# Performance work log

Measured on AMD Instinct MI355X. Metric: run time of the kernel, lower is better.

Reference implementation:

```python
import jax, jax.numpy as jnp
import numpy as np
import math

B = 1; SEQ = 2048; CHUNK = 16; K = SEQ // CHUNK
DIM = 1024; NH = 16; HD = DIM // NH
NL = 2; NLF = 2; HID = 4096; VOCAB = 32000; CSP_MAX = 4
EPS = 1e-5
BS = CHUNK + 2                 # per-chunk decoder block: [fx, sep, tokens]
L = K * BS + 2                 # + trailing [fx_last, sep]


def rope_cache(n_pos, n_elem, base=10000.0):
    theta = 1.0 / (base ** (jnp.arange(0, n_elem, 2, dtype=jnp.float32) / n_elem))
    idx = jnp.outer(jnp.arange(n_pos, dtype=jnp.float32), theta)  # [n_pos, n_elem/2]
    cos = jnp.concatenate([jnp.cos(idx), jnp.cos(idx)], -1)
    sin = jnp.concatenate([jnp.sin(idx), jnp.sin(idx)], -1)
    return cos, sin  # [n_pos, n_elem]


def apply_rope(x, cos, sin):
    # x: [b, h, l, d]; cos/sin: [l, d] (rope_n_elem == head_dim)
    h = x.shape[-1] // 2
    rot = jnp.concatenate([-x[..., h:], x[..., :h]], -1)
    return x * cos + rot * sin


def rmsnorm(x, w):
    return x * jax.lax.rsqrt(jnp.mean(x * x, -1, keepdims=True) + EPS) * w


def attention(x, wqkv, wo, cos, sin, mask):
    b, l, d = x.shape
    qkv = (x @ wqkv).reshape(b, l, 3, NH, HD).transpose(2, 0, 3, 1, 4)
    q, k, v = qkv[0], qkv[1], qkv[2]            # [b, h, l, hd]
    q = apply_rope(q, cos, sin)
    k = apply_rope(k, cos, sin)
    s = jnp.einsum('bhqd,bhkd->bhqk', q, k) / math.sqrt(HD)
    if mask is not None:
        s = jnp.where(mask, s, jnp.float32(-1e30))
    o = jnp.einsum('bhqk,bhkd->bhqd', jax.nn.softmax(s, -1), v)
    return o.transpose(0, 2, 1, 3).reshape(b, l, d) @ wo


def block(x, ln1, wqkv, wo, ln2, wg, wu, wd, cos, sin, mask):
    x = x + attention(rmsnorm(x, ln1), wqkv, wo, cos, sin, mask)
    h = rmsnorm(x, ln2)
    return x + (jax.nn.silu(h @ wg) * (h @ wu)) @ wd


def cat_mask(n, bs):
    # CAT mask: (kv divides block-start | same block) & causal
    q = jnp.arange(n)[:, None]
    kv = jnp.arange(n)[None, :]
    return ((kv % bs == 0) | (q // bs == kv // bs)) & (q >= kv)


def setup_inputs() -> dict:
    key = jax.random.key(0)
    ks = jax.random.split(key, 24)
    w = lambda k, s: jax.random.normal(k, s, jnp.float32) * 0.02
    return {
        'input_ids': jax.random.randint(ks[0], (B, SEQ), 0, VOCAB, dtype=jnp.int32),
        'chunk_size_power': 4,
        'f_wte': w(ks[1], (VOCAB, DIM)), 'f_pos': w(ks[2], (SEQ, DIM)),
        'f_adapt': w(ks[3], (CSP_MAX + 1, DIM)),
        'f_ln1': jnp.ones((NLF, DIM)), 'f_ln2': jnp.ones((NLF, DIM)),
        'f_wqkv': w(ks[4], (NLF, DIM, 3 * DIM)), 'f_wo': w(ks[5], (NLF, DIM, DIM)),
        'f_wg': w(ks[6], (NLF, DIM, HID)), 'f_wu': w(ks[7], (NLF, DIM, HID)),
        'f_wd': w(ks[8], (NLF, HID, DIM)),
        'f_norm': jnp.ones((DIM,)), 'f_proj': w(ks[9], (DIM, CHUNK * DIM)),
        'dummy_fx': w(ks[10], (CSP_MAX + 1, DIM)), 'wte': w(ks[11], (VOCAB, DIM)),
        'sep': w(ks[12], (1, DIM)),
        'd_ln1': jnp.ones((NL, DIM)), 'd_ln2': jnp.ones((NL, DIM)),
        'd_wqkv': w(ks[13], (NL, DIM, 3 * DIM)), 'd_wo': w(ks[14], (NL, DIM, DIM)),
        'd_wg': w(ks[15], (NL, DIM, HID)), 'd_wu': w(ks[16], (NL, DIM, HID)),
        'd_wd': w(ks[17], (NL, HID, DIM)),
        'd_norm': jnp.ones((DIM,)), 'w_out': w(ks[18], (VOCAB, DIM)),
    }


def reference(input_ids, chunk_size_power, f_wte, f_pos, f_adapt, f_ln1, f_ln2,
              f_wqkv, f_wo, f_wg, f_wu, f_wd, f_norm, f_proj, dummy_fx, wte, sep,
              d_ln1, d_ln2, d_wqkv, d_wo, d_wg, d_wu, d_wd, d_norm, w_out):
    csp = int(chunk_size_power)
    ids = input_ids.reshape(B, K, CHUNK)
    cosf, sinf = rope_cache(2 + CHUNK, HD)

    def compress(ids_c, chunk_idx):
        # ids_c: [B, CHUNK] (one chunk, vmapped over K)
        x = f_wte[ids_c]
        adaptive = jnp.broadcast_to(f_adapt[csp], (B, 1, DIM))
        pos_tok = jnp.broadcast_to(f_pos[chunk_idx], (B, 1, DIM))
        x = jnp.concatenate([adaptive, pos_tok, x], 1)  # [B, CHUNK+2, DIM]
        for i in range(NLF):
            x = block(x, f_ln1[i], f_wqkv[i], f_wo[i], f_ln2[i],
                      f_wg[i], f_wu[i], f_wd[i], cosf, sinf, None)
        x = rmsnorm(x, f_norm)[:, 2:, :].reshape(B, CHUNK * DIM)
        # chunk_size_power == log2(CHUNK): bilinear interpolate to same size == identity
        return x @ f_proj.T  # [B, DIM]

    fx = jax.vmap(compress, in_axes=(1, 0), out_axes=1)(ids, jnp.arange(K))  # [B, K, DIM]

    fx_last = fx[:, -1:, :]
    dummy = jnp.broadcast_to(dummy_fx[csp], (B, 1, DIM))
    fx_sh = jnp.concatenate([dummy, fx[:, :-1, :]], 1)[:, :, None, :]  # [B, K, 1, DIM]
    sep_t = jnp.broadcast_to(sep[0], (B, K, 1, DIM))
    emb = wte[ids]  # [B, K, CHUNK, DIM]
    x = jnp.concatenate([fx_sh, sep_t, emb], 2).reshape(B, K * BS, DIM)
    x = jnp.concatenate([x, fx_last, jnp.broadcast_to(sep[0], (B, 1, DIM))], 1)  # [B, L, DIM]

    # per-block repeating RoPE positions (cache built for len BS, tiled)
    pos = jnp.tile(jnp.arange(BS), K + 1)[:L]
    cosb, sinb = rope_cache(BS, HD)
    cosd, sind = cosb[pos], sinb[pos]
    mask = cat_mask(L, BS)

    for i in range(NL):
        x = block(x, d_ln1[i], d_wqkv[i], d_wo[i], d_ln2[i],
                  d_wg[i], d_wu[i], d_wd[i], cosd, sind, mask)
    x = rmsnorm(x, d_norm)
    return x @ w_out.T  # [B, L, VOCAB]
```

## Files before the change

kernel.cpp:

```cpp
#include <hip/hip_runtime.h>
#include <math.h>

#define L_DEC 2306
#define MPAD 2560
#define T_FINE 2304

typedef float f32x4 __attribute__((ext_vector_type(4)));
typedef __bf16 bf16x8 __attribute__((ext_vector_type(8)));
typedef unsigned short u16;
typedef unsigned short us4 __attribute__((ext_vector_type(4)));
typedef unsigned short us8 __attribute__((ext_vector_type(8)));

#define GLOAD16(g, l) __builtin_amdgcn_global_load_lds( \
    (const __attribute__((address_space(1))) unsigned int*)(g), \
    (__attribute__((address_space(3))) unsigned int*)(l), 16, 0, 0)

__device__ __forceinline__ u16 f2bf(float f) {
  unsigned u = __float_as_uint(f);
  u += 0x7fffu + ((u >> 16) & 1u);
  return (u16)(u >> 16);
}

__device__ __forceinline__ int fix_csp(const int* p) {
  int c = p[0];
  if ((unsigned)c <= 4u) return c;
  float f = __uint_as_float((unsigned)c);
  int c2 = (int)f;
  return ((unsigned)c2 <= 4u) ? c2 : 4;
}

__device__ __forceinline__ void xcd_map(int gx, int gy, int& bm, int& bn, int TS) {
  const int nwg = gx * gy;
  const int orig = blockIdx.y * gx + blockIdx.x;
  const int q8 = nwg >> 3, r8 = nwg & 7;
  const int xcd = orig & 7, idx8 = orig >> 3;
  const int wg = (xcd < r8 ? xcd * (q8 + 1) : r8 * (q8 + 1) + (xcd - r8) * q8) + idx8;
  bm = (wg / gx) * TS;
  bn = (wg % gx) * TS;
}

template<int EPI>
__global__ __launch_bounds__(512, 1) void k_gemm3(const u16* __restrict__ A,
                                                  const u16* __restrict__ B,
                                                  float* __restrict__ C,
                                                  int N, int K, int Mstore)
{
  extern __shared__ u16 lds[];
  const int tid = threadIdx.x;
  int bm, bn; xcd_map(gridDim.x, gridDim.y, bm, bn, 256);
  const int w = tid >> 6, lane = tid & 63;
  const int wm = (w >> 2) * 128, wn = (w & 3) * 64;
  const int lr = lane & 15, kh = lane >> 4;

#define STAGE3(buf, kt) do {                                                   \
    u16* lA = lds + (buf) * 32768;                                             \
    u16* lB = lA + 16384;                                                      \
    _Pragma("unroll")                                                          \
    for (int p = 0; p < 4; ++p) {                                              \
      int e = p * 512 + tid;                                                   \
      int row = e >> 3;                                                        \
      int kc = ((e & 7) ^ (row & 7)) * 8;    \
      GLOAD16(A + (size_t)(bm + row) * K + (size_t)(kt) * 64 + kc, lA + e * 8);\
      GLOAD16(B + (size_t)(bn + row) * K + (size_t)(kt) * 64 + kc, lB + e * 8);\
    }                                                                          \
  } while (0)

  f32x4 acc[8][4] = {};
  const int nt = K >> 6;
  STAGE3(0, 0);
  __syncthreads();
  int cur = 0;
  for (int t = 0; t < nt; ++t) {
    if (t + 1 < nt) STAGE3(cur ^ 1, t + 1);
    const u16* pA = lds + cur * 32768;
    const u16* pB = pA + 16384;
    const int xr = (lr & 7) << 3;
#pragma unroll
    for (int kt2 = 0; kt2 < 2; ++kt2) {
      bf16x8 af[8], bf[4];
#pragma unroll
      for (int m = 0; m < 8; ++m)
        af[m] = *(const bf16x8*)&pA[(wm + m * 16 + lr) * 64 + ((kt2 * 32 + kh * 8) ^ xr)];
#pragma unroll
      for (int n = 0; n < 4; ++n)
        bf[n] = *(const bf16x8*)&pB[(wn + n * 16 + lr) * 64 + ((kt2 * 32 + kh * 8) ^ xr)];
#pragma unroll
      for (int m = 0; m < 8; ++m)
#pragma unroll
        for (int n = 0; n < 4; ++n)
          acc[m][n] = __builtin_amdgcn_mfma_f32_16x16x32_bf16(af[m], bf[n], acc[m][n], 0, 0, 0);
    }
    __syncthreads();
    cur ^= 1;
  }
#undef STAGE3

#pragma unroll
  for (int m = 0; m < 8; ++m) {
    int gr0 = bm + wm + m * 16 + kh * 4;
#pragma unroll
    for (int n = 0; n < 4; ++n) {
      int gc = bn + wn + n * 16 + lr;
#pragma unroll
      for (int r = 0; r < 4; ++r) {
        int gr = gr0 + r;
        if (gr < Mstore) C[(size_t)gr * N + gc] = acc[m][n][r];
      }
    }
  }
}

template<int EPI>
__global__ __launch_bounds__(512, 1) void k_gemm2(const u16* __restrict__ A,
                                                  const u16* __restrict__ B,
                                                  float* __restrict__ C,
                                                  u16* __restrict__ Cb,
                                                  int N, int K, int Mstore)
{
  __shared__ u16 As[2][8192];
  __shared__ u16 Bs[2][8192];
  const int tid = threadIdx.x;
  int bm, bn; xcd_map(gridDim.x, gridDim.y, bm, bn, 256);
  const int w = tid >> 6, lane = tid & 63;
  const int wm = (w >> 2) * 128, wn = (w & 3) * 64;
  const int lr = lane & 15, kh = lane >> 4;
  const int r0 = tid >> 2;
  const int ksrc = 8 * ((tid & 3) ^ ((tid >> 3) & 3));
  const u16* ga = A + (size_t)(bm + r0) * K + ksrc;
  const u16* gb = B + (size_t)(bn + r0) * K + ksrc;
  const size_t rstep = (size_t)128 * K;
  const int cola = (kh * 8) ^ (((lr >> 1) & 3) << 3);

#define STAGE2(buf, kt) do {                                   \
    const u16* gA = ga + (size_t)(kt) * 32;                    \
    const u16* gB = gb + (size_t)(kt) * 32;                    \
    GLOAD16(gA,         &As[buf][tid * 8]);                    \
    GLOAD16(gA + rstep, &As[buf][tid * 8 + 4096]);             \
    GLOAD16(gB,         &Bs[buf][tid * 8]);                    \
    GLOAD16(gB + rstep, &Bs[buf][tid * 8 + 4096]);             \
  } while (0)

  f32x4 acc[8][4] = {};
  const int nt = K >> 5;
  STAGE2(0, 0);
  __syncthreads();
  int cur = 0;
  for (int t = 0; t < nt; ++t) {
    if (t + 1 < nt) STAGE2(cur ^ 1, t + 1);
    bf16x8 af[8], bf[4];
#pragma unroll
    for (int m = 0; m < 8; ++m)
      af[m] = *(const bf16x8*)&As[cur][(wm + m * 16 + lr) * 32 + cola];
#pragma unroll
    for (int n = 0; n < 4; ++n)
      bf[n] = *(const bf16x8*)&Bs[cur][(wn + n * 16 + lr) * 32 + cola];
#pragma unroll
    for (int m = 0; m < 8; ++m)
#pragma unroll
      for (int n = 0; n < 4; ++n)
        acc[m][n] = __builtin_amdgcn_mfma_f32_16x16x32_bf16(af[m], bf[n], acc[m][n], 0, 0, 0);
    __syncthreads();
    cur ^= 1;
  }
#undef STAGE2

#pragma unroll
  for (int m = 0; m < 8; ++m) {
    int gr0 = bm + wm + m * 16 + kh * 4;
#pragma unroll
    for (int n = 0; n < 4; ++n) {
      int gc = bn + wn + n * 16 + lr;
#pragma unroll
      for (int r = 0; r < 4; ++r) {
        int gr = gr0 + r;
        if (gr < Mstore) C[(size_t)gr * N + gc] = acc[m][n][r];
      }
    }
  }
}

template<int EPI>
__global__ __launch_bounds__(256) void k_gemm_bt(const u16* __restrict__ A,
                                                 const u16* __restrict__ B,
                                                 float* __restrict__ C,
                                                 u16* __restrict__ Cb,
                                                 int N, int K, int Mstore, int kchunk)
{
  __shared__ u16 As[4096];
  __shared__ u16 Bs[4096];
  const int tid = threadIdx.x;
  int bm, bn; xcd_map(gridDim.x, gridDim.y, bm, bn, 128);
  const int k0 = blockIdx.z * kchunk;
  const int w = tid >> 6, lane = tid & 63;
  const int wm = (w >> 1) * 64, wn = (w & 1) * 64;
  const int lr = lane & 15, kh = lane >> 4;
  const int r0 = tid >> 2;
  const int ksrc = 8 * ((tid & 3) ^ ((tid >> 3) & 3));
  const int cola = (kh * 8) ^ (((lr >> 1) & 3) << 3);

  const u16* ga = A + (size_t)(bm + r0) * K + k0 + ksrc;
  const u16* gb = B + (size_t)(bn + r0) * K + k0 + ksrc;
  u16* la = &As[tid * 8];
  u16* lb = &Bs[tid * 8];
  const size_t rstep = (size_t)64 * K;

  f32x4 acc[4][4] = {};
  for (int kk = 0; kk < kchunk; kk += 32) {
    GLOAD16(ga, la); GLOAD16(ga + rstep, la + 2048);
    GLOAD16(gb, lb); GLOAD16(gb + rstep, lb + 2048);
    ga += 32; gb += 32;
    __syncthreads();
    bf16x8 af[4], bfr[4];
#pragma unroll
    for (int m = 0; m < 4; ++m)
      af[m] = *(const bf16x8*)&As[(wm + m * 16 + lr) * 32 + cola];
#pragma unroll
    for (int n = 0; n < 4; ++n)
      bfr[n] = *(const bf16x8*)&Bs[(wn + n * 16 + lr) * 32 + cola];
#pragma unroll
    for (int m = 0; m < 4; ++m)
#pragma unroll
      for (int n = 0; n < 4; ++n)
        acc[m][n] = __builtin_amdgcn_mfma_f32_16x16x32_bf16(af[m], bfr[n], acc[m][n], 0, 0, 0);
    __syncthreads();
  }

  float* Cz = (EPI == 0) ? C + (size_t)blockIdx.z * Mstore * N : C;
  const int N2 = N >> 1;
#pragma unroll
  for (int m = 0; m < 4; ++m) {
    int gr0 = bm + wm + m * 16 + kh * 4;
#pragma unroll
    for (int n = 0; n < 4; ++n) {
      int gc = bn + wn + n * 16 + lr;
#pragma unroll
      for (int r = 0; r < 4; ++r) {
        int gr = gr0 + r;
        if (EPI == 2) {
          float x = acc[m][n][r];
          float px = __shfl_xor(x, 1);
          if (!(lr & 1) && gr < Mstore) {
            float s = x / (1.f + expf(-x)) * px;
            Cb[(size_t)gr * N2 + (gc >> 1)] = f2bf(s);
          }
        } else if (gr < Mstore) {
          size_t off = (size_t)gr * N + gc;
          if (EPI == 0) Cz[off] = acc[m][n][r];
          else          C[off] += acc[m][n][r];
        }
      }
    }
  }
}

__global__ __launch_bounds__(256) void k_gemm_hf(const u16* __restrict__ A,
                                                 const float* __restrict__ B,
                                                 float* __restrict__ C,
                                                 int N, int K, int Mstore)
{
  __shared__ u16 As[4096];
  __shared__ u16 Bs[4096];
  const int tid = threadIdx.x;
  const int bm = blockIdx.y * 128, bn = blockIdx.x * 128;
  const int w = tid >> 6, lane = tid & 63;
  const int wm = (w >> 1) * 64, wn = (w & 1) * 64;
  const int lr = lane & 15, kh = lane >> 4;
  const int r0 = tid >> 2;
  const int ksrc = 8 * ((tid & 3) ^ ((tid >> 3) & 3));
  const int cola = (kh * 8) ^ (((lr >> 1) & 3) << 3);
  const u16* ga = A + (size_t)(bm + r0) * K + ksrc;
  u16* la = &As[tid * 8];
  const size_t rstep = (size_t)64 * K;

  f32x4 acc[4][4] = {};
  for (int kk = 0; kk < K; kk += 32) {
    GLOAD16(ga, la); GLOAD16(ga + rstep, la + 2048);
    ga += 32;
#pragma unroll
    for (int p = 0; p < 4; ++p) {
      int e = tid + p * 256;
      int row = e >> 3, kc = (e & 7) * 4;
      int kcs = kc ^ (((row >> 1) & 3) << 3);
      float4 v = *(const float4*)(B + (size_t)(bn + row) * K + kk + kc);
      us4 pk; pk[0] = f2bf(v.x); pk[1] = f2bf(v.y); pk[2] = f2bf(v.z); pk[3] = f2bf(v.w);
      *(us4*)&Bs[row * 32 + kcs] = pk;
    }
    __syncthreads();
    bf16x8 af[4], bfr[4];
#pragma unroll
    for (int m = 0; m < 4; ++m)
      af[m] = *(const bf16x8*)&As[(wm + m * 16 + lr) * 32 + cola];
#pragma unroll
    for (int n = 0; n < 4; ++n)
      bfr[n] = *(const bf16x8*)&Bs[(wn + n * 16 + lr) * 32 + cola];
#pragma unroll
    for (int m = 0; m < 4; ++m)
#pragma unroll
      for (int n = 0; n < 4; ++n)
        acc[m][n] = __builtin_amdgcn_mfma_f32_16x16x32_bf16(af[m], bfr[n], acc[m][n], 0, 0, 0);
    __syncthreads();
  }
#pragma unroll
  for (int m = 0; m < 4; ++m) {
    int gr0 = bm + wm + m * 16 + kh * 4;
#pragma unroll
    for (int n = 0; n < 4; ++n) {
      int gc = bn + wn + n * 16 + lr;
#pragma unroll
      for (int r = 0; r < 4; ++r) {
        int gr = gr0 + r;
        if (gr < Mstore) C[(size_t)gr * N + gc] = acc[m][n][r];
      }
    }
  }
}

__global__ __launch_bounds__(256) void k_wt2(const float* __restrict__ W, u16* __restrict__ Wt,
                                             int K, int N, int rs, int ro) {
  __shared__ u16 t[64][80];
  int n0 = blockIdx.x * 64, k0 = blockIdx.y * 64;
#pragma unroll
  for (int p = 0; p < 4; ++p) {
    int id = threadIdx.x + p * 256;
    int row = id >> 4, c4 = (id & 15) * 4;
    float4 v = *(const float4*)(W + (size_t)(k0 + row) * N + n0 + c4);
    t[c4 + 0][row] = f2bf(v.x);
    t[c4 + 1][row] = f2bf(v.y);
    t[c4 + 2][row] = f2bf(v.z);
    t[c4 + 3][row] = f2bf(v.w);
  }
  __syncthreads();
#pragma unroll
  for (int p = 0; p < 2; ++p) {
    int id = threadIdx.x + p * 256;
    int row = id >> 3, c8 = (id & 7) * 8;
    *(us8*)(Wt + ((size_t)(n0 + row) * rs + ro) * K + k0 + c8) = *(const us8*)&t[row][c8];
  }
}

__global__ void k_cvt(const float* __restrict__ x, u16* __restrict__ y, int n4) {
  for (int i = blockIdx.x * 256 + threadIdx.x; i < n4; i += gridDim.x * 256) {
    float4 v = ((const float4*)x)[i];
    us4 p; p[0] = f2bf(v.x); p[1] = f2bf(v.y); p[2] = f2bf(v.z); p[3] = f2bf(v.w);
    ((us4*)y)[i] = p;
  }
}

__global__ void k_reduce_add(const float* __restrict__ p, float* __restrict__ dst,
                             int n, int planes, int addDst) {
  for (int i = blockIdx.x * 256 + threadIdx.x; i < n; i += gridDim.x * 256) {
    float s = addDst ? dst[i] : 0.f;
    for (int z = 0; z < planes; ++z) s += p[(size_t)z * n + i];
    dst[i] = s;
  }
}

__global__ void k_rope_table(float* __restrict__ cosT, float* __restrict__ sinT) {
  int i = blockIdx.x * blockDim.x + threadIdx.x;
  if (i >= 18 * 64) return;
  int p = i >> 6, d = i & 63;
  float theta = powf(10000.f, -(float)(d & 31) / 32.f);
  float ang = (float)p * theta;
  cosT[i] = cosf(ang);
  sinT[i] = sinf(ang);
}

__global__ void k_fine_embed(const int* __restrict__ ids, const int* __restrict__ cspp,
                             const float* __restrict__ f_wte, const float* __restrict__ f_pos,
                             const float* __restrict__ f_adapt, float* __restrict__ xF) {
  int csp = fix_csp(cspp);
  for (int idx = blockIdx.x * 256 + threadIdx.x; idx < T_FINE * 1024; idx += gridDim.x * 256) {
    int r = idx >> 10, d = idx & 1023;
    int c = r / 18, j = r - c * 18;
    float v;
    if (j == 0)      v = f_adapt[csp * 1024 + d];
    else if (j == 1) v = f_pos[c * 1024 + d];
    else             v = f_wte[(size_t)ids[c * 16 + j - 2] * 1024 + d];
    xF[idx] = v;
  }
}

__global__ __launch_bounds__(256) void k_rmsnorm_bf(const float* __restrict__ x,
                                                    const float* __restrict__ w,
                                                    u16* __restrict__ y) {
  int t = blockIdx.x;
  const float4 v = *(const float4*)(x + (size_t)t * 1024 + threadIdx.x * 4);
  float ss = v.x * v.x + v.y * v.y + v.z * v.z + v.w * v.w;
#pragma unroll
  for (int off = 32; off; off >>= 1) ss += __shfl_xor(ss, off);
  __shared__ float ps[4];
  if ((threadIdx.x & 63) == 0) ps[threadIdx.x >> 6] = ss;
  __syncthreads();
  float inv = rsqrtf((ps[0] + ps[1] + ps[2] + ps[3]) * (1.f / 1024.f) + 1e-5f);
  const float4 wv = *(const float4*)(w + threadIdx.x * 4);
  us4 o;
  o[0] = f2bf(v.x * inv * wv.x); o[1] = f2bf(v.y * inv * wv.y);
  o[2] = f2bf(v.z * inv * wv.z); o[3] = f2bf(v.w * inv * wv.w);
  *(us4*)(y + (size_t)t * 1024 + threadIdx.x * 4) = o;
}

__global__ __launch_bounds__(256) void k_rmsnorm_pack_bf(const float* __restrict__ x,
                                                         const float* __restrict__ w,
                                                         u16* __restrict__ y) {
  int b = blockIdx.x;
  int c = b >> 4, r = b & 15;
  const float* xr = x + (size_t)(c * 18 + 2 + r) * 1024;
  const float4 v = *(const float4*)(xr + threadIdx.x * 4);
  float ss = v.x * v.x + v.y * v.y + v.z * v.z + v.w * v.w;
#pragma unroll
  for (int off = 32; off; off >>= 1) ss += __shfl_xor(ss, off);
  __shared__ float ps[4];
  if ((threadIdx.x & 63) == 0) ps[threadIdx.x >> 6] = ss;
  __syncthreads();
  float inv = rsqrtf((ps[0] + ps[1] + ps[2] + ps[3]) * (1.f / 1024.f) + 1e-5f);
  const float4 wv = *(const float4*)(w + threadIdx.x * 4);
  us4 o;
  o[0] = f2bf(v.x * inv * wv.x); o[1] = f2bf(v.y * inv * wv.y);
  o[2] = f2bf(v.z * inv * wv.z); o[3] = f2bf(v.w * inv * wv.w);
  *(us4*)(y + (size_t)b * 1024 + threadIdx.x * 4) = o;
}

__global__ __launch_bounds__(256) void k_rope(float* __restrict__ qkv,
                                              const float* __restrict__ cosT,
                                              const float* __restrict__ sinT) {
  int t = blockIdx.x;
  int p = t % 18;
  float* row = qkv + (size_t)t * 3072;
#pragma unroll
  for (int i = 0; i < 4; ++i) {
    int it = threadIdx.x + i * 256;
    int s = it >> 9, rem = it & 511, h = rem >> 5, d = rem & 31;
    float* px = row + s * 1024 + h * 64 + d;
    float x1 = px[0], x2 = px[32];
    float cv = cosT[p * 64 + d], sv = sinT[p * 64 + d];
    px[0]  = x1 * cv - x2 * sv;
    px[32] = x2 * cv + x1 * sv;
  }
}

__global__ __launch_bounds__(256) void k_attn_fine2(const float* __restrict__ qkv,
                                                    u16* __restrict__ out) {
  __shared__ float q[4][18][68], k[4][18][68], v[4][18][68], s[4][18][20];
  int c = blockIdx.x;
  int w = threadIdx.x >> 6, lane = threadIdx.x & 63;
  int h = blockIdx.y * 4 + w;
  const float* base = qkv + (size_t)c * 18 * 3072 + h * 64;
#pragma unroll 3
  for (int r = 0; r < 18; ++r) {
    q[w][r][lane] = base[(size_t)r * 3072 + lane];
    k[w][r][lane] = base[(size_t)r * 3072 + 1024 + lane];
    v[w][r][lane] = base[(size_t)r * 3072 + 2048 + lane];
  }
  __syncthreads();
#pragma unroll
  for (int it = 0; it < 6; ++it) {
    int idx = lane + it * 64;
    if (idx < 324) {
      int qi = (idx * 3641) >> 16;
      int ki = idx - qi * 18;
      const float* qr = q[w][qi];
      const float* kr = k[w][ki];
      float a = 0.f;
#pragma unroll
      for (int d = 0; d < 64; d += 4) {
        float4 x = *(const float4*)&qr[d];
        float4 y = *(const float4*)&kr[d];
        a += x.x * y.x + x.y * y.y + x.z * y.z + x.w * y.w;
      }
      s[w][qi][ki] = a * 0.125f;
    }
  }
  __syncthreads();
  if (lane < 18) {
    float mx = -1e30f;
#pragma unroll
    for (int j = 0; j < 18; ++j) mx = fmaxf(mx, s[w][lane][j]);
    float sum = 0.f;
#pragma unroll
    for (int j = 0; j < 18; ++j) { float e = expf(s[w][lane][j] - mx); s[w][lane][j] = e; sum += e; }
    float inv = 1.f / sum;
#pragma unroll
    for (int j = 0; j < 18; ++j) s[w][lane][j] *= inv;
  }
  __syncthreads();
  float vcol[18];
#pragma unroll
  for (int ki = 0; ki < 18; ++ki) vcol[ki] = v[w][ki][lane];
#pragma unroll 2
  for (int qi = 0; qi < 18; ++qi) {
    float o = 0.f;
#pragma unroll
    for (int ki = 0; ki < 18; ++ki) o += s[w][qi][ki] * vcol[ki];
    out[(size_t)(c * 18 + qi) * 1024 + h * 64 + lane] = f2bf(o);
  }
}

__global__ __launch_bounds__(512) void k_attn_dec3(const float* __restrict__ qkv,
                                                   u16* __restrict__ out) {
  extern __shared__ float dyn[];
  float* Kl = dyn;
  float* Vl = Kl + 146 * 65;
  float* Ql = Vl + 146 * 65;
  float* Sw = Ql + 18 * 65;
  const int bq = blockIdx.x, h = blockIdx.y;
  const int w = threadIdx.x >> 6, lane = threadIdx.x & 63;
  const int t0 = 18 * bq;
  const int nq = (bq < 128) ? 18 : 2;
  const int nstage = (bq < 128) ? (bq + 18) : 130;

  {
    int rr = threadIdx.x >> 2, c = threadIdx.x & 3;
    for (int row = rr; row < nstage; row += 128) {
      int kv = (row <= bq) ? 18 * row : t0 + (row - bq);
      const float* kp = qkv + (size_t)kv * 3072 + 1024 + h * 64 + c * 16;
#pragma unroll
      for (int q4 = 0; q4 < 4; ++q4) {
        float4 a = *(const float4*)(kp + q4 * 4);
        float4 b = *(const float4*)(kp + 1024 + q4 * 4);
        int d = c * 16 + q4 * 4;
        float* kd = Kl + row * 65 + d;
        float* vd = Vl + row * 65 + d;
        kd[0] = a.x; kd[1] = a.y; kd[2] = a.z; kd[3] = a.w;
        vd[0] = b.x; vd[1] = b.y; vd[2] = b.z; vd[3] = b.w;
      }
    }
    if (rr < nq) {
      const float* qp = qkv + (size_t)(t0 + rr) * 3072 + h * 64 + c * 16;
#pragma unroll
      for (int q4 = 0; q4 < 4; ++q4) {
        float4 a = *(const float4*)(qp + q4 * 4);
        int d = c * 16 + q4 * 4;
        float* qd = Ql + rr * 65 + d;
        qd[0] = a.x; qd[1] = a.y; qd[2] = a.z; qd[3] = a.w;
      }
    }
  }
  __syncthreads();

  for (int r = w; r < nq; r += 8) {
    const int nk = bq + 1 + r;
    float* S = Sw + w * 148;
    const float* qr = Ql + r * 65;
    float mx = -1e30f;
    for (int i = lane; i < nk; i += 64) {
      const float* kr = Kl + i * 65;
      float a = 0.f;
#pragma unroll
      for (int d = 0; d < 64; ++d) a += qr[d] * kr[d];
      a *= 0.125f;
      S[i] = a;
      mx = fmaxf(mx, a);
    }
#pragma unroll
    for (int off = 32; off; off >>= 1) mx = fmaxf(mx, __shfl_xor(mx, off));
    float sum = 0.f;
    for (int i = lane; i < nk; i += 64) { float e = expf(S[i] - mx); S[i] = e; sum += e; }
#pragma unroll
    for (int off = 32; off; off >>= 1) sum += __shfl_xor(sum, off);
    float inv = 1.f / sum;
    __builtin_amdgcn_wave_barrier();
    float o = 0.f;
    for (int i = 0; i < nk; ++i) o += S[i] * Vl[i * 65 + lane];
    out[(size_t)(t0 + r) * 1024 + h * 64 + lane] = f2bf(o * inv);
  }
}

__global__ __launch_bounds__(256) void k_attn_dec2(const float* __restrict__ qkv,
                                                   u16* __restrict__ out) {
  __shared__ float sc_s[4][160];
  int t = blockIdx.x;
  int w = threadIdx.x >> 6, lane = threadIdx.x & 63;
  int h = blockIdx.y * 4 + w;
  float* sc = sc_s[w];
  int bq = t / 18;
  int nstart = bq + 1;
  int nown = t - 18 * bq;
  int nk = nstart + nown;
  int g = lane >> 2, j = lane & 3;
  const float* qb = qkv + (size_t)t * 3072 + h * 64 + j * 16;
  float4 q0 = *(const float4*)(qb);
  float4 q1 = *(const float4*)(qb + 4);
  float4 q2 = *(const float4*)(qb + 8);
  float4 q3 = *(const float4*)(qb + 12);
  for (int i0 = 0; i0 < nk; i0 += 16) {
    int i = i0 + g;
    float p = 0.f;
    if (i < nk) {
      int kv = (i < nstart) ? 18 * i : 18 * bq + (i - nstart) + 1;
      const float* kp = qkv + (size_t)kv * 3072 + 1024 + h * 64 + j * 16;
      float4 k0 = *(const float4*)(kp);
      float4 k1 = *(const float4*)(kp + 4);
      float4 k2 = *(const float4*)(kp + 8);
      float4 k3 = *(const float4*)(kp + 12);
      p = q0.x * k0.x + q0.y * k0.y + q0.z * k0.z + q0.w * k0.w
        + q1.x * k1.x + q1.y * k1.y + q1.z * k1.z + q1.w * k1.w
        + q2.x * k2.x + q2.y * k2.y + q2.z * k2.z + q2.w * k2.w
        + q3.x * k3.x + q3.y * k3.y + q3.z * k3.z + q3.w * k3.w;
    }
    p += __shfl_xor(p, 1);
    p += __shfl_xor(p, 2);
    if (i < nk && j == 0) sc[i] = p * 0.125f;
  }
  __syncthreads();
  float mx = -1e30f;
  for (int i = lane; i < nk; i += 64) mx = fmaxf(mx, sc[i]);
#pragma unroll
  for (int off = 32; off; off >>= 1) mx = fmaxf(mx, __shfl_xor(mx, off));
  float sum = 0.f;
  for (int i = lane; i < nk; i += 64) { float e = expf(sc[i] - mx); sc[i] = e; sum += e; }
#pragma unroll
  for (int off = 32; off; off >>= 1) sum += __shfl_xor(sum, off);
  float inv = 1.f / sum;
  __syncthreads();
  const float* vb = qkv + 2048 + h * 64 + lane;
  float o0 = 0.f, o1 = 0.f, o2 = 0.f, o3 = 0.f;
  int i = 0;
  for (; i + 4 <= nk; i += 4) {
    int ia = i, ib = i + 1, ic = i + 2, id = i + 3;
    int kva = (ia < nstart) ? 18 * ia : 18 * bq + (ia - nstart) + 1;
    int kvb = (ib < nstart) ? 18 * ib : 18 * bq + (ib - nstart) + 1;
    int kvc = (ic < nstart) ? 18 * ic : 18 * bq + (ic - nstart) + 1;
    int kvd = (id < nstart) ? 18 * id : 18 * bq + (id - nstart) + 1;
    o0 += sc[ia] * vb[(size_t)kva * 3072];
    o1 += sc[ib] * vb[(size_t)kvb * 3072];
    o2 += sc[ic] * vb[(size_t)kvc * 3072];
    o3 += sc[id] * vb[(size_t)kvd * 3072];
  }
  for (; i < nk; ++i) {
    int kv = (i < nstart) ? 18 * i : 18 * bq + (i - nstart) + 1;
    o0 += sc[i] * vb[(size_t)kv * 3072];
  }
  float o = (o0 + o1) + (o2 + o3);
  out[(size_t)t * 1024 + h * 64 + lane] = f2bf(o * inv);
}

__global__ void k_assemble(const int* __restrict__ ids, const int* __restrict__ cspp,
                           const float* __restrict__ fx, const float* __restrict__ dummy_fx,
                           const float* __restrict__ sep, const float* __restrict__ wte,
                           float* __restrict__ xD) {
  int csp = fix_csp(cspp);
  for (int idx = blockIdx.x * 256 + threadIdx.x; idx < MPAD * 1024; idx += gridDim.x * 256) {
    int t = idx >> 10, d = idx & 1023;
    float v;
    if (t >= L_DEC)     v = 0.f;
    else if (t == 2305) v = sep[d];
    else if (t == 2304) v = fx[127 * 1024 + d];
    else {
      int k = t / 18, r = t - k * 18;
      if (r == 0)      v = (k == 0) ? dummy_fx[csp * 1024 + d] : fx[(k - 1) * 1024 + d];
      else if (r == 1) v = sep[d];
      else             v = wte[(size_t)ids[k * 16 + r - 2] * 1024 + d];
    }
    xD[idx] = v;
  }
}

extern "C" void kernel_launch(void* const* d_in, const int* in_sizes, int n_in,
                              void* d_out, int out_size, void* d_ws, size_t ws_size,
                              hipStream_t stream) {
  const int*   input_ids = (const int*)d_in[0];
  const int*   cspp      = (const int*)d_in[1];
  const float* f_wte     = (const float*)d_in[2];
  const float* f_pos     = (const float*)d_in[3];
  const float* f_adapt   = (const float*)d_in[4];
  const float* f_ln1     = (const float*)d_in[5];
  const float* f_ln2     = (const float*)d_in[6];
  const float* f_wqkv    = (const float*)d_in[7];
  const float* f_wo      = (const float*)d_in[8];
  const float* f_wg      = (const float*)d_in[9];
  const float* f_wu      = (const float*)d_in[10];
  const float* f_wd      = (const float*)d_in[11];
  const float* f_norm    = (const float*)d_in[12];
  const float* f_proj    = (const float*)d_in[13];
  const float* dummy_fx  = (const float*)d_in[14];
  const float* wte       = (const float*)d_in[15];
  const float* sep       = (const float*)d_in[16];
  const float* d_ln1     = (const float*)d_in[17];
  const float* d_ln2     = (const float*)d_in[18];
  const float* d_wqkv    = (const float*)d_in[19];
  const float* d_wo      = (const float*)d_in[20];
  const float* d_wg      = (const float*)d_in[21];
  const float* d_wu      = (const float*)d_in[22];
  const float* d_wd      = (const float*)d_in[23];
  const float* d_norm    = (const float*)d_in[24];
  const float* w_out     = (const float*)d_in[25];

  float* cosT = (float*)d_ws;
  float* sinT = cosT + 1152;
  u16*   bufH = (u16*)(sinT + 1152);
  u16*   w_outb = bufH + (size_t)MPAD * 1024;
  const size_t WS_NEED = 2 * 1152 * 4 + (size_t)MPAD * 1024 * 2 + (size_t)32000 * 1024 * 2;
  const bool big_ws = ws_size >= WS_NEED;

  float* o       = (float*)d_out;
  float* xF      = o;
  float* xD      = xF + (size_t)T_FINE * 1024;
  float* fx      = xD + (size_t)MPAD * 1024;
  float* bufQKV  = fx + 128 * 1024;
  u16*   bufA    = (u16*)(bufQKV + (size_t)MPAD * 3072);
  u16*   bufGb   = bufA + (size_t)MPAD * 1024;
  u16*   packedb = bufGb + (size_t)MPAD * 4096;
  u16*   Wt      = packedb + (size_t)128 * 16384;
  u16*   projb   = Wt + (size_t)8192 * 1024;
  float* spk     = (float*)(projb + (size_t)1024 * 16384);

  const size_t ATTN_LDS = (size_t)(146 * 65 * 2 + 18 * 65 + 8 * 148) * 4;
  hipError_t eattn = hipFuncSetAttribute(
      reinterpret_cast<const void*>(&k_attn_dec3),
      hipFuncAttributeMaxDynamicSharedMemorySize, (int)ATTN_LDS);

#define GEMM_BT(EPI, Ap, Bp, Cp, Cbp, Mpad, N, K, Mstore, S) \
  k_gemm_bt<EPI><<<dim3((N) / 128, (Mpad) / 128, (S)), 256, 0, stream>>>((Ap), (Bp), (Cp), (Cbp), (N), (K), (Mstore), (K) / (S))

  k_rope_table<<<5, 256, 0, stream>>>(cosT, sinT);
  k_fine_embed<<<2048, 256, 0, stream>>>(input_ids, cspp, f_wte, f_pos, f_adapt, xF);

  for (int i = 0; i < 2; ++i) {
    k_rmsnorm_bf<<<T_FINE, 256, 0, stream>>>(xF, f_ln1 + i * 1024, bufH);
    k_wt2<<<dim3(48, 16), 256, 0, stream>>>(f_wqkv + (size_t)i * 1024 * 3072, Wt, 1024, 3072, 1, 0);
    GEMM_BT(0, bufH, Wt, bufQKV, (u16*)nullptr, T_FINE, 3072, 1024, T_FINE, 1);
    k_rope<<<T_FINE, 256, 0, stream>>>(bufQKV, cosT, sinT);
    k_attn_fine2<<<dim3(128, 4), 256, 0, stream>>>(bufQKV, bufA);
    k_wt2<<<dim3(16, 16), 256, 0, stream>>>(f_wo + (size_t)i * 1024 * 1024, Wt, 1024, 1024, 1, 0);
    GEMM_BT(1, bufA, Wt, xF, (u16*)nullptr, T_FINE, 1024, 1024, T_FINE, 1);
    k_rmsnorm_bf<<<T_FINE, 256, 0, stream>>>(xF, f_ln2 + i * 1024, bufH);
    k_wt2<<<dim3(64, 16), 256, 0, stream>>>(f_wg + (size_t)i * 1024 * 4096, Wt, 1024, 4096, 2, 0);
    k_wt2<<<dim3(64, 16), 256, 0, stream>>>(f_wu + (size_t)i * 1024 * 4096, Wt, 1024, 4096, 2, 1);
    GEMM_BT(2, bufH, Wt, (float*)nullptr, bufGb, T_FINE, 8192, 1024, T_FINE, 1);
    k_wt2<<<dim3(16, 64), 256, 0, stream>>>(f_wd + (size_t)i * 4096 * 1024, Wt, 4096, 1024, 1, 0);
    GEMM_BT(0, bufGb, Wt, spk, (u16*)nullptr, T_FINE, 1024, 4096, T_FINE, 4);
    k_reduce_add<<<2048, 256, 0, stream>>>(spk, xF, T_FINE * 1024, 4, 1);
  }

  k_rmsnorm_pack_bf<<<2048, 256, 0, stream>>>(xF, f_norm, packedb);
  k_cvt<<<2048, 256, 0, stream>>>(f_proj, projb, 1024 * 16384 / 4);
  GEMM_BT(0, packedb, projb, spk, (u16*)nullptr, 128, 1024, 16384, 128, 32);
  k_reduce_add<<<512, 256, 0, stream>>>(spk, fx, 128 * 1024, 32, 0);

  k_assemble<<<2048, 256, 0, stream>>>(input_ids, cspp, fx, dummy_fx, sep, wte, xD);
  for (int i = 0; i < 2; ++i) {
    k_rmsnorm_bf<<<MPAD, 256, 0, stream>>>(xD, d_ln1 + i * 1024, bufH);
    k_wt2<<<dim3(48, 16), 256, 0, stream>>>(d_wqkv + (size_t)i * 1024 * 3072, Wt, 1024, 3072, 1, 0);
    GEMM_BT(0, bufH, Wt, bufQKV, (u16*)nullptr, MPAD, 3072, 1024, MPAD, 1);
    k_rope<<<L_DEC, 256, 0, stream>>>(bufQKV, cosT, sinT);
    if (eattn == hipSuccess) {
      k_attn_dec3<<<dim3(129, 16), 512, ATTN_LDS, stream>>>(bufQKV, bufA);
    } else {
      k_attn_dec2<<<dim3(L_DEC, 4), 256, 0, stream>>>(bufQKV, bufA);
    }
    k_wt2<<<dim3(16, 16), 256, 0, stream>>>(d_wo + (size_t)i * 1024 * 1024, Wt, 1024, 1024, 1, 0);
    GEMM_BT(1, bufA, Wt, xD, (u16*)nullptr, MPAD, 1024, 1024, MPAD, 1);
    k_rmsnorm_bf<<<MPAD, 256, 0, stream>>>(xD, d_ln2 + i * 1024, bufH);
    k_wt2<<<dim3(64, 16), 256, 0, stream>>>(d_wg + (size_t)i * 1024 * 4096, Wt, 1024, 4096, 2, 0);
    k_wt2<<<dim3(64, 16), 256, 0, stream>>>(d_wu + (size_t)i * 1024 * 4096, Wt, 1024, 4096, 2, 1);
    GEMM_BT(2, bufH, Wt, (float*)nullptr, bufGb, MPAD, 8192, 1024, MPAD, 1);
    k_wt2<<<dim3(16, 64), 256, 0, stream>>>(d_wd + (size_t)i * 4096 * 1024, Wt, 4096, 1024, 1, 0);
    GEMM_BT(0, bufGb, Wt, spk, (u16*)nullptr, MPAD, 1024, 4096, MPAD, 4);
    k_reduce_add<<<2048, 256, 0, stream>>>(spk, xD, MPAD * 1024, 4, 1);
  }

  k_rmsnorm_bf<<<MPAD, 256, 0, stream>>>(xD, d_norm, bufH);
  if (big_ws) {
    k_cvt<<<2048, 256, 0, stream>>>(w_out, w_outb, 32000 * 1024 / 4);
    hipError_t ae = hipFuncSetAttribute(
        reinterpret_cast<const void*>(&k_gemm3<0>),
        hipFuncAttributeMaxDynamicSharedMemorySize, 131072);
    if (ae == hipSuccess) {
      k_gemm3<0><<<dim3(125, 10), 512, 131072, stream>>>(bufH, w_outb, o, 32000, 1024, L_DEC);
    } else {
      k_gemm2<0><<<dim3(125, 10), 512, 0, stream>>>(bufH, w_outb, o, nullptr, 32000, 1024, L_DEC);
    }
  } else {
    k_gemm_hf<<<dim3(250, MPAD / 128), 256, 0, stream>>>(bufH, w_out, o, 32000, 1024, L_DEC);
  }
#undef GEMM_BT
}
```

Baseline: 1.504 ms.

## Fuse RoPE into QKV GEMM epilogue and residual-add into RMSNorm kernels

Removes the separate RoPE kernel by applying rotary embedding in a new QKV GEMM epilogue. It replaces reduce-add plus RMSNorm pairs with a single k_red_norm kernel that sums split-K planes, updates the residual and emits the normalized bf16 activations. The Wo GEMM now runs split-K into planes instead of read-modify-write, and the gate/up weight conversions are merged into one launch. The big output GEMM switches to a column-major tile mapping. These changes cut launches and global-memory round trips of the activation tensors, at the cost of extra epilogue work and more complex code.

```diff
diff --git a/kernel.cpp b/kernel.cpp
--- a/kernel.cpp
+++ b/kernel.cpp
@@ -29,14 +29,15 @@
   return ((unsigned)c2 <= 4u) ? c2 : 4;
 }
 
+template<int ROWMAJ>
 __device__ __forceinline__ void xcd_map(int gx, int gy, int& bm, int& bn, int TS) {
   const int nwg = gx * gy;
   const int orig = blockIdx.y * gx + blockIdx.x;
   const int q8 = nwg >> 3, r8 = nwg & 7;
   const int xcd = orig & 7, idx8 = orig >> 3;
   const int wg = (xcd < r8 ? xcd * (q8 + 1) : r8 * (q8 + 1) + (xcd - r8) * q8) + idx8;
-  bm = (wg / gx) * TS;
-  bn = (wg % gx) * TS;
+  if (ROWMAJ) { bm = (wg / gx) * TS; bn = (wg % gx) * TS; }
+  else        { bm = (wg % gy) * TS; bn = (wg / gy) * TS; }
 }
 
 template<int EPI>
@@ -47,7 +48,7 @@
 {
   extern __shared__ u16 lds[];
   const int tid = threadIdx.x;
-  int bm, bn; xcd_map(gridDim.x, gridDim.y, bm, bn, 256);
+  int bm, bn; xcd_map<0>(gridDim.x, gridDim.y, bm, bn, 256);
   const int w = tid >> 6, lane = tid & 63;
   const int wm = (w >> 2) * 128, wn = (w & 3) * 64;
   const int lr = lane & 15, kh = lane >> 4;
@@ -120,7 +121,7 @@
   __shared__ u16 As[2][8192];
   __shared__ u16 Bs[2][8192];
   const int tid = threadIdx.x;
-  int bm, bn; xcd_map(gridDim.x, gridDim.y, bm, bn, 256);
+  int bm, bn; xcd_map<1>(gridDim.x, gridDim.y, bm, bn, 256);
   const int w = tid >> 6, lane = tid & 63;
   const int wm = (w >> 2) * 128, wn = (w & 3) * 64;
   const int lr = lane & 15, kh = lane >> 4;
@@ -184,12 +185,14 @@
                                                  const u16* __restrict__ B,
                                                  float* __restrict__ C,
                                                  u16* __restrict__ Cb,
+                                                 const float* __restrict__ cosT,
+                                                 const float* __restrict__ sinT,
                                                  int N, int K, int Mstore, int kchunk)
 {
   __shared__ u16 As[4096];
   __shared__ u16 Bs[4096];
   const int tid = threadIdx.x;
-  int bm, bn; xcd_map(gridDim.x, gridDim.y, bm, bn, 128);
+  int bm, bn; xcd_map<1>(gridDim.x, gridDim.y, bm, bn, 128);
   const int k0 = blockIdx.z * kchunk;
   const int w = tid >> 6, lane = tid & 63;
   const int wm = (w >> 1) * 64, wn = (w & 1) * 64;
@@ -227,26 +230,51 @@
 
   float* Cz = (EPI == 0) ? C + (size_t)blockIdx.z * Mstore * N : C;
   const int N2 = N >> 1;
+  const bool doRope = (EPI == 3) && ((bn + wn) < 2048);
 #pragma unroll
   for (int m = 0; m < 4; ++m) {
     int gr0 = bm + wm + m * 16 + kh * 4;
 #pragma unroll
-    for (int n = 0; n < 4; ++n) {
-      int gc = bn + wn + n * 16 + lr;
-#pragma unroll
-      for (int r = 0; r < 4; ++r) {
-        int gr = gr0 + r;
-        if (EPI == 2) {
+    for (int r = 0; r < 4; ++r) {
+      int gr = gr0 + r;
+      if (EPI == 3) {
+        int p = gr % 18;
+        if (doRope) {
+#pragma unroll
+          for (int n2 = 0; n2 < 2; ++n2) {
+            int d = n2 * 16 + lr;
+            float c = cosT[p * 64 + d], s = sinT[p * 64 + d];
+            float x1 = acc[m][n2][r], x2 = acc[m][n2 + 2][r];
+            if (gr < Mstore) {
+              int gc = bn + wn + n2 * 16 + lr;
+              C[(size_t)gr * N + gc]      = x1 * c - x2 * s;
+              C[(size_t)gr * N + gc + 32] = x2 * c + x1 * s;
+            }
+          }
+        } else if (gr < Mstore) {
+#pragma unroll
+          for (int n = 0; n < 4; ++n)
+            C[(size_t)gr * N + bn + wn + n * 16 + lr] = acc[m][n][r];
+        }
+      } else if (EPI == 2) {
+#pragma unroll
+        for (int n = 0; n < 4; ++n) {
           float x = acc[m][n][r];
           float px = __shfl_xor(x, 1);
           if (!(lr & 1) && gr < Mstore) {
-            float s = x / (1.f + expf(-x)) * px;
-            Cb[(size_t)gr * N2 + (gc >> 1)] = f2bf(s);
+            int gc = bn + wn + n * 16 + lr;
+            float sgl = x / (1.f + expf(-x)) * px;
+            Cb[(size_t)gr * N2 + (gc >> 1)] = f2bf(sgl);
           }
-        } else if (gr < Mstore) {
-          size_t off = (size_t)gr * N + gc;
-          if (EPI == 0) Cz[off] = acc[m][n][r];
-          else          C[off] += acc[m][n][r];
+        }
+      } else {
+        if (gr < Mstore) {
+#pragma unroll
+          for (int n = 0; n < 4; ++n) {
+            size_t off = (size_t)gr * N + bn + wn + n * 16 + lr;
+            if (EPI == 0) Cz[off] = acc[m][n][r];
+            else          C[off] += acc[m][n][r];
+          }
         }
       }
     }
@@ -315,15 +343,19 @@
   }
 }
 
-__global__ __launch_bounds__(256) void k_wt2(const float* __restrict__ W, u16* __restrict__ Wt,
+__global__ __launch_bounds__(256) void k_wt2(const float* __restrict__ W,
+                                             const float* __restrict__ W2,
+                                             u16* __restrict__ Wt,
                                              int K, int N, int rs, int ro) {
   __shared__ u16 t[64][80];
+  const float* src = (blockIdx.z == 0) ? W : W2;
+  int roz = ro + blockIdx.z;
   int n0 = blockIdx.x * 64, k0 = blockIdx.y * 64;
 #pragma unroll
   for (int p = 0; p < 4; ++p) {
     int id = threadIdx.x + p * 256;
     int row = id >> 4, c4 = (id & 15) * 4;
-    float4 v = *(const float4*)(W + (size_t)(k0 + row) * N + n0 + c4);
+    float4 v = *(const float4*)(src + (size_t)(k0 + row) * N + n0 + c4);
     t[c4 + 0][row] = f2bf(v.x);
     t[c4 + 1][row] = f2bf(v.y);
     t[c4 + 2][row] = f2bf(v.z);
@@ -334,7 +366,7 @@
   for (int p = 0; p < 2; ++p) {
     int id = threadIdx.x + p * 256;
     int row = id >> 3, c8 = (id & 7) * 8;
-    *(us8*)(Wt + ((size_t)(n0 + row) * rs + ro) * K + k0 + c8) = *(const us8*)&t[row][c8];
+    *(us8*)(Wt + ((size_t)(n0 + row) * rs + roz) * K + k0 + c8) = *(const us8*)&t[row][c8];
   }
 }
 
@@ -352,6 +384,37 @@
     float s = addDst ? dst[i] : 0.f;
     for (int z = 0; z < planes; ++z) s += p[(size_t)z * n + i];
     dst[i] = s;
+  }
+}
+
+template<int S, int NORM>
+__global__ __launch_bounds__(256) void k_red_norm(const float* __restrict__ planes,
+                                                  float* __restrict__ x,
+                                                  const float* __restrict__ w,
+                                                  u16* __restrict__ y) {
+  const int t = blockIdx.x;
+  const int n = gridDim.x * 1024;
+  const size_t base = (size_t)t * 1024 + threadIdx.x * 4;
+  float4 a = *(const float4*)(x + base);
+#pragma unroll
+  for (int s = 0; s < S; ++s) {
+    float4 p = *(const float4*)(planes + (size_t)s * n + base);
+    a.x += p.x; a.y += p.y; a.z += p.z; a.w += p.w;
+  }
+  *(float4*)(x + base) = a;
+  if (NORM) {
+    float ss = a.x * a.x + a.y * a.y + a.z * a.z + a.w * a.w;
+#pragma unroll
+    for (int off = 32; off; off >>= 1) ss += __shfl_xor(ss, off);
+    __shared__ float ps[4];
+    if ((threadIdx.x & 63) == 0) ps[threadIdx.x >> 6] = ss;
+    __syncthreads();
+    float inv = rsqrtf((ps[0] + ps[1] + ps[2] + ps[3]) * (1.f / 1024.f) + 1e-5f);
+    const float4 wv = *(const float4*)(w + threadIdx.x * 4);
+    us4 o;
+    o[0] = f2bf(a.x * inv * wv.x); o[1] = f2bf(a.y * inv * wv.y);
+    o[2] = f2bf(a.z * inv * wv.z); o[3] = f2bf(a.w * inv * wv.w);
+    *(us4*)(y + base) = o;
   }
 }
 
@@ -418,24 +481,6 @@
   o[0] = f2bf(v.x * inv * wv.x); o[1] = f2bf(v.y * inv * wv.y);
   o[2] = f2bf(v.z * inv * wv.z); o[3] = f2bf(v.w * inv * wv.w);
   *(us4*)(y + (size_t)b * 1024 + threadIdx.x * 4) = o;
-}
-
-__global__ __launch_bounds__(256) void k_rope(float* __restrict__ qkv,
-                                              const float* __restrict__ cosT,
-                                              const float* __restrict__ sinT) {
-  int t = blockIdx.x;
-  int p = t % 18;
-  float* row = qkv + (size_t)t * 3072;
-#pragma unroll
-  for (int i = 0; i < 4; ++i) {
-    int it = threadIdx.x + i * 256;
-    int s = it >> 9, rem = it & 511, h = rem >> 5, d = rem & 31;
-    float* px = row + s * 1024 + h * 64 + d;
-    float x1 = px[0], x2 = px[32];
-    float cv = cosT[p * 64 + d], sv = sinT[p * 64 + d];
-    px[0]  = x1 * cv - x2 * sv;
-    px[32] = x2 * cv + x1 * sv;
-  }
 }
 
 __global__ __launch_bounds__(256) void k_attn_fine2(const float* __restrict__ qkv,
@@ -710,26 +755,27 @@
       hipFuncAttributeMaxDynamicSharedMemorySize, (int)ATTN_LDS);
 
 #define GEMM_BT(EPI, Ap, Bp, Cp, Cbp, Mpad, N, K, Mstore, S) \
-  k_gemm_bt<EPI><<<dim3((N) / 128, (Mpad) / 128, (S)), 256, 0, stream>>>((Ap), (Bp), (Cp), (Cbp), (N), (K), (Mstore), (K) / (S))
+  k_gemm_bt<EPI><<<dim3((N) / 128, (Mpad) / 128, (S)), 256, 0, stream>>>((Ap), (Bp), (Cp), (Cbp), cosT, sinT, (N), (K), (Mstore), (K) / (S))
+#define WT1(Wp, Kd, Nd) k_wt2<<<dim3((Nd) / 64, (Kd) / 64, 1), 256, 0, stream>>>((Wp), nullptr, Wt, (Kd), (Nd), 1, 0)
 
   k_rope_table<<<5, 256, 0, stream>>>(cosT, sinT);
   k_fine_embed<<<2048, 256, 0, stream>>>(input_ids, cspp, f_wte, f_pos, f_adapt, xF);
+  k_rmsnorm_bf<<<T_FINE, 256, 0, stream>>>(xF, f_ln1, bufH);
 
   for (int i = 0; i < 2; ++i) {
-    k_rmsnorm_bf<<<T_FINE, 256, 0, stream>>>(xF, f_ln1 + i * 1024, bufH);
-    k_wt2<<<dim3(48, 16), 256, 0, stream>>>(f_wqkv + (size_t)i * 1024 * 3072, Wt, 1024, 3072, 1, 0);
-    GEMM_BT(0, bufH, Wt, bufQKV, (u16*)nullptr, T_FINE, 3072, 1024, T_FINE, 1);
-    k_rope<<<T_FINE, 256, 0, stream>>>(bufQKV, cosT, sinT);
+    WT1(f_wqkv + (size_t)i * 1024 * 3072, 1024, 3072);
+    GEMM_BT(3, bufH, Wt, bufQKV, (u16*)nullptr, T_FINE, 3072, 1024, T_FINE, 1);
     k_attn_fine2<<<dim3(128, 4), 256, 0, stream>>>(bufQKV, bufA);
-    k_wt2<<<dim3(16, 16), 256, 0, stream>>>(f_wo + (size_t)i * 1024 * 1024, Wt, 1024, 1024, 1, 0);
-    GEMM_BT(1, bufA, Wt, xF, (u16*)nullptr, T_FINE, 1024, 1024, T_FINE, 1);
-    k_rmsnorm_bf<<<T_FINE, 256, 0, stream>>>(xF, f_ln2 + i * 1024, bufH);
-    k_wt2<<<dim3(64, 16), 256, 0, stream>>>(f_wg + (size_t)i * 1024 * 4096, Wt, 1024, 4096, 2, 0);
-    k_wt2<<<dim3(64, 16), 256, 0, stream>>>(f_wu + (size_t)i * 1024 * 4096, Wt, 1024, 4096, 2, 1);
+    WT1(f_wo + (size_t)i * 1024 * 1024, 1024, 1024);
+    GEMM_BT(0, bufA, Wt, spk, (u16*)nullptr, T_FINE, 1024, 1024, T_FINE, 2);
+    k_red_norm<2, 1><<<T_FINE, 256, 0, stream>>>(spk, xF, f_ln2 + i * 1024, bufH);
+    k_wt2<<<dim3(64, 16, 2), 256, 0, stream>>>(f_wg + (size_t)i * 1024 * 4096,
+                                               f_wu + (size_t)i * 1024 * 4096, Wt, 1024, 4096, 2, 0);
     GEMM_BT(2, bufH, Wt, (float*)nullptr, bufGb, T_FINE, 8192, 1024, T_FINE, 1);
-    k_wt2<<<dim3(16, 64), 256, 0, stream>>>(f_wd + (size_t)i * 4096 * 1024, Wt, 4096, 1024, 1, 0);
+    WT1(f_wd + (size_t)i * 4096 * 1024, 4096, 1024);
     GEMM_BT(0, bufGb, Wt, spk, (u16*)nullptr, T_FINE, 1024, 4096, T_FINE, 4);
-    k_reduce_add<<<2048, 256, 0, stream>>>(spk, xF, T_FINE * 1024, 4, 1);
+    if (i == 0) k_red_norm<4, 1><<<T_FINE, 256, 0, stream>>>(spk, xF, f_ln1 + 1024, bufH);
+    else        k_red_norm<4, 0><<<T_FINE, 256, 0, stream>>>(spk, xF, nullptr, nullptr);
   }
 
   k_rmsnorm_pack_bf<<<2048, 256, 0, stream>>>(xF, f_norm, packedb);
@@ -738,28 +784,27 @@
   k_reduce_add<<<512, 256, 0, stream>>>(spk, fx, 128 * 1024, 32, 0);
 
   k_assemble<<<2048, 256, 0, stream>>>(input_ids, cspp, fx, dummy_fx, sep, wte, xD);
+  k_rmsnorm_bf<<<MPAD, 256, 0, stream>>>(xD, d_ln1, bufH);
   for (int i = 0; i < 2; ++i) {
-    k_rmsnorm_bf<<<MPAD, 256, 0, stream>>>(xD, d_ln1 + i * 1024, bufH);
-    k_wt2<<<dim3(48, 16), 256, 0, stream>>>(d_wqkv + (size_t)i * 1024 * 3072, Wt, 1024, 3072, 1, 0);
-    GEMM_BT(0, bufH, Wt, bufQKV, (u16*)nullptr, MPAD, 3072, 1024, MPAD, 1);
-    k_rope<<<L_DEC, 256, 0, stream>>>(bufQKV, cosT, sinT);
+    WT1(d_wqkv + (size_t)i * 1024 * 3072, 1024, 3072);
+    GEMM_BT(3, bufH, Wt, bufQKV, (u16*)nullptr, MPAD, 3072, 1024, MPAD, 1);
     if (eattn == hipSuccess) {
       k_attn_dec3<<<dim3(129, 16), 512, ATTN_LDS, stream>>>(bufQKV, bufA);
     } else {
       k_attn_dec2<<<dim3(L_DEC, 4), 256, 0, stream>>>(bufQKV, bufA);
     }
-    k_wt2<<<dim3(16, 16), 256, 0, stream>>>(d_wo + (size_t)i * 1024 * 1024, Wt, 1024, 1024, 1, 0);
-    GEMM_BT(1, bufA, Wt, xD, (u16*)nullptr, MPAD, 1024, 1024, MPAD, 1);
-    k_rmsnorm_bf<<<MPAD, 256, 0, stream>>>(xD, d_ln2 + i * 1024, bufH);
-    k_wt2<<<dim3(64, 16), 256, 0, stream>>>(d_wg + (size_t)i * 1024 * 4096, Wt, 1024, 4096, 2, 0);
-    k_wt2<<<dim3(64, 16), 256, 0, stream>>>(d_wu + (size_t)i * 1024 * 4096, Wt, 1024, 4096, 2, 1);
+    WT1(d_wo + (size_t)i * 1024 * 1024, 1024, 1024);
+    GEMM_BT(0, bufA, Wt, spk, (u16*)nullptr, MPAD, 1024, 1024, MPAD, 2);
+    k_red_norm<2, 1><<<MPAD, 256, 0, stream>>>(spk, xD, d_ln2 + i * 1024, bufH);
+    k_wt2<<<dim3(64, 16, 2), 256, 0, stream>>>(d_wg + (size_t)i * 1024 * 4096,
+                                               d_wu + (size_t)i * 1024 * 4096, Wt, 1024, 4096, 2, 0);
     GEMM_BT(2, bufH, Wt, (float*)nullptr, bufGb, MPAD, 8192, 1024, MPAD, 1);
-    k_wt2<<<dim3(16, 64), 256, 0, stream>>>(d_wd + (size_t)i * 4096 * 1024, Wt, 4096, 1024, 1, 0);
+    WT1(d_wd + (size_t)i * 4096 * 1024, 4096, 1024);
     GEMM_BT(0, bufGb, Wt, spk, (u16*)nullptr, MPAD, 1024, 4096, MPAD, 4);
-    k_reduce_add<<<2048, 256, 0, stream>>>(spk, xD, MPAD * 1024, 4, 1);
-  }
-
-  k_rmsnorm_bf<<<MPAD, 256, 0, stream>>>(xD, d_norm, bufH);
+    const float* nw = (i == 0) ? d_ln1 + 1024 : d_norm;
+    k_red_norm<4, 1><<<MPAD, 256, 0, stream>>>(spk, xD, nw, bufH);
+  }
+
   if (big_ws) {
     k_cvt<<<2048, 256, 0, stream>>>(w_out, w_outb, 32000 * 1024 / 4);
     hipError_t ae = hipFuncSetAttribute(
@@ -773,5 +818,6 @@
   } else {
     k_gemm_hf<<<dim3(250, MPAD / 128), 256, 0, stream>>>(bufH, w_out, o, 32000, 1024, L_DEC);
   }
+#undef WT1
 #undef GEMM_BT
 }
```

Result: faster. 1.387 ms (-7.7%).
